# Optimization experiments

Measured on AMD Instinct MI355X. Metric: run time of the kernel, lower is better.

The kernel has to match this reference:

```python
import jax, jax.numpy as jnp
import numpy as np

WINDOW = 8
NUM_HEADS = 16


def setup_inputs() -> dict:
    key = jax.random.key(0)
    k1, k2, k3 = jax.random.split(key, 3)
    B, N_actual, C = 2048, 60, 512
    inputs = jax.random.normal(k1, (B, N_actual, C), dtype=jnp.float32)
    qkv_w = jax.random.normal(k2, (C, 3 * C), dtype=jnp.float32) * 0.05
    qkv_b = jnp.zeros((3 * C,), dtype=jnp.float32)
    proj_w = jax.random.normal(k3, (C, C), dtype=jnp.float32) * 0.05
    proj_b = jnp.zeros((C,), dtype=jnp.float32)
    return {"inputs": inputs, "qkv_w": qkv_w, "qkv_b": qkv_b, "proj_w": proj_w, "proj_b": proj_b}


def reference(inputs, qkv_w, qkv_b, proj_w, proj_b):
    B, N_actual, C = inputs.shape
    H = NUM_HEADS
    hd = C // H
    Nw = WINDOW * WINDOW  # num_tokens_in_window = 64
    pad = Nw - N_actual
    scale = hd ** -0.5

    # pad tokens up to the window size and build the internal padding mask
    x = jnp.pad(inputs, ((0, 0), (0, pad), (0, 0)))  # [B, Nw, C]
    mask = jnp.concatenate(
        [jnp.ones((B, N_actual), dtype=x.dtype), jnp.zeros((B, pad), dtype=x.dtype)], axis=1
    )  # [B, Nw]

    # fused QKV projection
    qkv = x @ qkv_w + qkv_b  # [B, Nw, 3C]
    qkv = qkv.reshape(B, Nw, 3, H, hd).transpose(2, 0, 3, 1, 4)  # [3, B, H, Nw, hd]
    q, k, v = qkv[0] * scale, qkv[1], qkv[2]

    # scaled dot-product attention with additive padding mask
    scores = jnp.einsum("bhnd,bhmd->bhnm", q, k)  # [B, H, Nw, Nw]
    additive_mask = (1.0 - mask)[:, None, None, :] * jnp.asarray(-1e9, scores.dtype)
    attn = jax.nn.softmax(scores + additive_mask, axis=-1)

    out = jnp.einsum("bhnm,bhmd->bhnd", attn, v)  # [B, H, Nw, hd]
    out = out.transpose(0, 2, 1, 3).reshape(B, Nw, C)
    out = out @ proj_w + proj_b
    return out[:, :N_actual, :]
```

## Files before the change

### kernel.cpp

```cpp
#include <hip/hip_runtime.h>

typedef __bf16 bf16x8 __attribute__((ext_vector_type(8)));
typedef float  f32x4  __attribute__((ext_vector_type(4)));

__device__ __forceinline__ f32x4 mfma16(bf16x8 a, bf16x8 b, f32x4 c) {
    return __builtin_amdgcn_mfma_f32_16x16x32_bf16(a, b, c, 0, 0, 0);
}

__device__ __forceinline__ unsigned bpack2(float a, float b) {
    union { __bf16 h[2]; unsigned u; } z;
    z.h[0] = (__bf16)a; z.h[1] = (__bf16)b;
    return z.u;
}

__global__ void kprep(const float* __restrict__ qkvw, const float* __restrict__ qkvb,
                      const float* __restrict__ projw,
                      __bf16* __restrict__ wqkv_t, __bf16* __restrict__ wp_t,
                      float* __restrict__ bias_eff)
{
    const float s = 0.17677669529663687f;
    int idx = blockIdx.x * 256 + threadIdx.x;
    if (idx < 786432) {
        int c = idx >> 9, k = idx & 511;
        float v = qkvw[k * 1536 + c];
        if (c < 512) v *= s;
        wqkv_t[idx] = (__bf16)v;
    } else if (idx < 1048576) {
        int j = idx - 786432;
        int c = j >> 9, k = j & 511;
        wp_t[j] = (__bf16)projw[k * 512 + c];
    } else if (idx < 1050112) {
        int c = idx - 1048576;
        float v = qkvb[c];
        if (c < 512) v *= s;
        bias_eff[c] = v;
    }
}

__global__ __launch_bounds__(512, 2) void kfused8(
    const float*  __restrict__ xin,
    const __bf16* __restrict__ wqkv,
    const float*  __restrict__ bias_eff,
    const __bf16* __restrict__ wp,
    const float*  __restrict__ projb,
    float*        __restrict__ out)
{
    const int b    = blockIdx.x;
    const int tid  = threadIdx.x;
    const int lane = tid & 63;
    const int w    = tid >> 6;
    const int q4   = lane >> 4;
    const int l15  = lane & 15;

    extern __shared__ char smem[];
    char* xs = smem;
    char* wb = smem + 65536 + w * 12288;

    const f32x4 fzero = {0.f, 0.f, 0.f, 0.f};

#pragma unroll
    for (int j = 0; j < 8; ++j) {
        int ci = j * 512 + tid;
        int r  = ci >> 6;
        int k0 = (ci & 63) << 3;
        float4 f0 = make_float4(0.f, 0.f, 0.f, 0.f), f1 = f0;
        if (r < 60) {
            const float4* s4 = reinterpret_cast<const float4*>(
                xin + ((size_t)b * 60 + r) * 512 + k0);
            f0 = s4[0]; f1 = s4[1];
        }
        bf16x8 v;
        v[0]=(__bf16)f0.x; v[1]=(__bf16)f0.y; v[2]=(__bf16)f0.z; v[3]=(__bf16)f0.w;
        v[4]=(__bf16)f1.x; v[5]=(__bf16)f1.y; v[6]=(__bf16)f1.z; v[7]=(__bf16)f1.w;
        int addr = ((((k0 >> 5) << 2) + (r >> 4)) * 64
                    + ((k0 >> 3) & 3) * 16 + (r & 15)) * 16;
        *reinterpret_cast<bf16x8*>(xs + addr) = v;
    }
    __syncthreads();

    unsigned oA[16], oB[16];

    for (int i = 0; i < 2; ++i) {
        const int h = (w << 1) + i;
        __threadfence_block();

        for (int s = 0; s < 3; ++s) {
            const __bf16* wcol = wqkv + ((size_t)(s * 512 + h * 32 + l15) * 512) + q4 * 8;
            f32x4 acc[4][2];
#pragma unroll
            for (int mt = 0; mt < 4; ++mt)
#pragma unroll
                for (int n = 0; n < 2; ++n) acc[mt][n] = fzero;

#pragma unroll
            for (int kk = 0; kk < 16; ++kk) {
                bf16x8 a[4];
#pragma unroll
                for (int mt = 0; mt < 4; ++mt)
                    a[mt] = *reinterpret_cast<const bf16x8*>(
                        xs + (((kk << 2) + mt) * 64 + lane) * 16);
                bf16x8 bw[2];
#pragma unroll
                for (int n = 0; n < 2; ++n)
                    bw[n] = *reinterpret_cast<const bf16x8*>(
                        wcol + (size_t)(n * 16) * 512 + kk * 32);
#pragma unroll
                for (int mt = 0; mt < 4; ++mt)
#pragma unroll
                    for (int n = 0; n < 2; ++n)
                        acc[mt][n] = mfma16(a[mt], bw[n], acc[mt][n]);
            }
            float bs0 = bias_eff[s * 512 + h * 32 + l15];
            float bs1 = bias_eff[s * 512 + h * 32 + 16 + l15];
#pragma unroll
            for (int mt = 0; mt < 4; ++mt)
#pragma unroll
                for (int n = 0; n < 2; ++n)
#pragma unroll
                    for (int reg = 0; reg < 4; ++reg) {
                        float val = acc[mt][n][reg] + (n ? bs1 : bs0);
                        if (s < 2) {
                            int hd = n * 16 + l15;
                            int addr = s * 4096
                                + ((mt * 64 + (hd >> 3) * 16 + q4 * 4 + reg) * 16)
                                + (hd & 7) * 2;
                            *reinterpret_cast<__bf16*>(wb + addr) = (__bf16)val;
                        } else {
                            int key = mt * 16 + q4 * 4 + reg;
                            int g   = ((mt >> 1) << 1) + n;
                            int addr = 8192
                                + ((g * 64 + ((key >> 3) & 3) * 16 + l15) * 16)
                                + (key & 7) * 2;
                            *reinterpret_cast<__bf16*>(wb + addr) = (__bf16)val;
                        }
                    }
        }
        __threadfence_block();

        bf16x8 qa[4], kb[4];
#pragma unroll
        for (int mt = 0; mt < 4; ++mt)
            qa[mt] = *reinterpret_cast<const bf16x8*>(wb + (mt * 64 + lane) * 16);
#pragma unroll
        for (int nt = 0; nt < 4; ++nt)
            kb[nt] = *reinterpret_cast<const bf16x8*>(wb + 4096 + (nt * 64 + lane) * 16);
        f32x4 sc[4][4];
#pragma unroll
        for (int mt = 0; mt < 4; ++mt)
#pragma unroll
            for (int nt = 0; nt < 4; ++nt)
                sc[mt][nt] = mfma16(qa[mt], kb[nt], fzero);

        float inv_rs[4][4];
#pragma unroll
        for (int mt = 0; mt < 4; ++mt)
#pragma unroll
            for (int reg = 0; reg < 4; ++reg) {
                float m0 = fmaxf(fmaxf(sc[mt][0][reg], sc[mt][1][reg]), sc[mt][2][reg]);
                float v3 = (l15 < 12) ? sc[mt][3][reg] : -3.0e38f;
                m0 = fmaxf(m0, v3);
#pragma unroll
                for (int d = 1; d < 16; d <<= 1)
                    m0 = fmaxf(m0, __shfl_xor(m0, d));
                float ssum = 0.f;
#pragma unroll
                for (int nt = 0; nt < 4; ++nt) {
                    float p = (nt == 3 && l15 >= 12) ? 0.f
                              : __expf(sc[mt][nt][reg] - m0);
                    sc[mt][nt][reg] = p;
                    ssum += p;
                }
#pragma unroll
                for (int d = 1; d < 16; d <<= 1)
                    ssum += __shfl_xor(ssum, d);
                inv_rs[mt][reg] = 1.f / ssum;
            }

#pragma unroll
        for (int mt = 0; mt < 4; ++mt)
#pragma unroll
            for (int nt = 0; nt < 4; ++nt)
#pragma unroll
                for (int reg = 0; reg < 4; ++reg) {
                    int addr = (((((nt >> 1) << 2) + mt) * 64)
                                + ((((nt & 1) << 1) + (l15 >> 3)) * 16 + q4 * 4 + reg)) * 16
                               + (l15 & 7) * 2;
                    *reinterpret_cast<__bf16*>(wb + addr) = (__bf16)sc[mt][nt][reg];
                }
        __threadfence_block();

        bf16x8 pa[4][2], vb[2][2];
#pragma unroll
        for (int mt = 0; mt < 4; ++mt)
#pragma unroll
            for (int ks = 0; ks < 2; ++ks)
                pa[mt][ks] = *reinterpret_cast<const bf16x8*>(
                    wb + (((ks << 2) + mt) * 64 + lane) * 16);
#pragma unroll
        for (int ks = 0; ks < 2; ++ks)
#pragma unroll
            for (int n = 0; n < 2; ++n)
                vb[ks][n] = *reinterpret_cast<const bf16x8*>(
                    wb + 8192 + (((ks << 1) + n) * 64 + lane) * 16);
        f32x4 o[4][2];
#pragma unroll
        for (int mt = 0; mt < 4; ++mt)
#pragma unroll
            for (int n = 0; n < 2; ++n) {
                o[mt][n] = mfma16(pa[mt][0], vb[0][n], fzero);
                o[mt][n] = mfma16(pa[mt][1], vb[1][n], o[mt][n]);
            }

#pragma unroll
        for (int mt = 0; mt < 4; ++mt)
#pragma unroll
            for (int n = 0; n < 2; ++n)
#pragma unroll
                for (int rp = 0; rp < 2; ++rp) {
                    unsigned pk = bpack2(o[mt][n][2 * rp]     * inv_rs[mt][2 * rp],
                                         o[mt][n][2 * rp + 1] * inv_rs[mt][2 * rp + 1]);
                    if (i == 0) oA[mt * 4 + n * 2 + rp] = pk;
                    else        oB[mt * 4 + n * 2 + rp] = pk;
                }
    }

    __syncthreads();
    {
        const int h0 = w << 1;
#pragma unroll
        for (int mt = 0; mt < 4; ++mt)
#pragma unroll
            for (int n = 0; n < 2; ++n)
#pragma unroll
                for (int rp = 0; rp < 2; ++rp) {
                    int s0 = ((((h0 << 2) + mt) * 64)
                              + ((n * 2 + (l15 >> 3)) * 16 + q4 * 4 + rp * 2)) * 16
                             + (l15 & 7) * 2;
                    unsigned pa = oA[mt * 4 + n * 2 + rp];
                    unsigned pb = oB[mt * 4 + n * 2 + rp];
                    *reinterpret_cast<unsigned short*>(xs + s0)           = (unsigned short)pa;
                    *reinterpret_cast<unsigned short*>(xs + s0 + 16)      = (unsigned short)(pa >> 16);
                    *reinterpret_cast<unsigned short*>(xs + s0 + 4096)    = (unsigned short)pb;
                    *reinterpret_cast<unsigned short*>(xs + s0 + 4096+16) = (unsigned short)(pb >> 16);
                }
    }
    __syncthreads();

    float* outp = out + (size_t)b * 30720;
    for (int pass = 0; pass < 2; ++pass) {
        const int nt0 = (w << 2) + (pass << 1);
        f32x4 acc[4][2];
#pragma unroll
        for (int mt = 0; mt < 4; ++mt)
#pragma unroll
            for (int n = 0; n < 2; ++n) acc[mt][n] = fzero;

#pragma unroll
        for (int kk = 0; kk < 16; ++kk) {
            bf16x8 a[4];
#pragma unroll
            for (int mt = 0; mt < 4; ++mt)
                a[mt] = *reinterpret_cast<const bf16x8*>(
                    xs + (((kk << 2) + mt) * 64 + lane) * 16);
            bf16x8 bw[2];
#pragma unroll
            for (int n = 0; n < 2; ++n)
                bw[n] = *reinterpret_cast<const bf16x8*>(
                    wp + (size_t)((nt0 + n) * 16 + l15) * 512 + kk * 32 + q4 * 8);
#pragma unroll
            for (int mt = 0; mt < 4; ++mt)
#pragma unroll
                for (int n = 0; n < 2; ++n)
                    acc[mt][n] = mfma16(a[mt], bw[n], acc[mt][n]);
        }
#pragma unroll
        for (int n = 0; n < 2; ++n) {
            int c = (nt0 + n) * 16 + l15;
            float bias = projb[c];
#pragma unroll
            for (int mt = 0; mt < 4; ++mt)
#pragma unroll
                for (int reg = 0; reg < 4; ++reg) {
                    int row = mt * 16 + q4 * 4 + reg;
                    if (row < 60)
                        outp[row * 512 + c] = acc[mt][n][reg] + bias;
                }
        }
    }
}

__global__ __launch_bounds__(256, 1) void ka_fused(
    const float*  __restrict__ xin,
    const __bf16* __restrict__ wqkv,
    const float*  __restrict__ bias_eff,
    char*         __restrict__ aobase)
{
    const int b    = blockIdx.x;
    const int tid  = threadIdx.x;
    const int lane = tid & 63;
    const int w    = tid >> 6;
    const int q4   = lane >> 4;
    const int l15  = lane & 15;

    extern __shared__ char smem[];
    char* xs = smem;
    char* wb = smem + 65536 + w * 12288;

    const f32x4 fzero = {0.f, 0.f, 0.f, 0.f};

#pragma unroll
    for (int j = 0; j < 16; ++j) {
        int ci = j * 256 + tid;
        int r  = ci >> 6;
        int k0 = (ci & 63) << 3;
        float4 f0 = make_float4(0.f, 0.f, 0.f, 0.f), f1 = f0;
        if (r < 60) {
            const float4* s4 = reinterpret_cast<const float4*>(
                xin + ((size_t)b * 60 + r) * 512 + k0);
            f0 = s4[0]; f1 = s4[1];
        }
        bf16x8 v;
        v[0]=(__bf16)f0.x; v[1]=(__bf16)f0.y; v[2]=(__bf16)f0.z; v[3]=(__bf16)f0.w;
        v[4]=(__bf16)f1.x; v[5]=(__bf16)f1.y; v[6]=(__bf16)f1.z; v[7]=(__bf16)f1.w;
        int addr = ((((k0 >> 5) << 2) + (r >> 4)) * 64
                    + ((k0 >> 3) & 3) * 16 + (r & 15)) * 16;
        *reinterpret_cast<bf16x8*>(xs + addr) = v;
    }
    __syncthreads();

    for (int i = 0; i < 4; ++i) {
        const int h = (w << 2) + i;
        __threadfence_block();

        for (int s = 0; s < 3; ++s) {
            const __bf16* wcol = wqkv + ((size_t)(s * 512 + h * 32 + l15) * 512) + q4 * 8;
            f32x4 acc[4][2];
#pragma unroll
            for (int mt = 0; mt < 4; ++mt)
#pragma unroll
                for (int n = 0; n < 2; ++n) acc[mt][n] = fzero;

#pragma unroll
            for (int kk = 0; kk < 16; ++kk) {
                bf16x8 a[4];
#pragma unroll
                for (int mt = 0; mt < 4; ++mt)
                    a[mt] = *reinterpret_cast<const bf16x8*>(
                        xs + (((kk << 2) + mt) * 64 + lane) * 16);
                bf16x8 bw[2];
#pragma unroll
                for (int n = 0; n < 2; ++n)
                    bw[n] = *reinterpret_cast<const bf16x8*>(
                        wcol + (size_t)(n * 16) * 512 + kk * 32);
#pragma unroll
                for (int mt = 0; mt < 4; ++mt)
#pragma unroll
                    for (int n = 0; n < 2; ++n)
                        acc[mt][n] = mfma16(a[mt], bw[n], acc[mt][n]);
            }
            float bs0 = bias_eff[s * 512 + h * 32 + l15];
            float bs1 = bias_eff[s * 512 + h * 32 + 16 + l15];
#pragma unroll
            for (int mt = 0; mt < 4; ++mt)
#pragma unroll
                for (int n = 0; n < 2; ++n)
#pragma unroll
                    for (int reg = 0; reg < 4; ++reg) {
                        float val = acc[mt][n][reg] + (n ? bs1 : bs0);
                        if (s < 2) {
                            int hd = n * 16 + l15;
                            int addr = s * 4096
                                + ((mt * 64 + (hd >> 3) * 16 + q4 * 4 + reg) * 16)
                                + (hd & 7) * 2;
                            *reinterpret_cast<__bf16*>(wb + addr) = (__bf16)val;
                        } else {
                            int key = mt * 16 + q4 * 4 + reg;
                            int g   = ((mt >> 1) << 1) + n;
                            int addr = 8192
                                + ((g * 64 + ((key >> 3) & 3) * 16 + l15) * 16)
                                + (key & 7) * 2;
                            *reinterpret_cast<__bf16*>(wb + addr) = (__bf16)val;
                        }
                    }
        }
        __threadfence_block();

        bf16x8 qa[4], kb[4];
#pragma unroll
        for (int mt = 0; mt < 4; ++mt)
            qa[mt] = *reinterpret_cast<const bf16x8*>(wb + (mt * 64 + lane) * 16);
#pragma unroll
        for (int nt = 0; nt < 4; ++nt)
            kb[nt] = *reinterpret_cast<const bf16x8*>(wb + 4096 + (nt * 64 + lane) * 16);
        f32x4 sc[4][4];
#pragma unroll
        for (int mt = 0; mt < 4; ++mt)
#pragma unroll
            for (int nt = 0; nt < 4; ++nt)
                sc[mt][nt] = mfma16(qa[mt], kb[nt], fzero);

        float inv_rs[4][4];
#pragma unroll
        for (int mt = 0; mt < 4; ++mt)
#pragma unroll
            for (int reg = 0; reg < 4; ++reg) {
                float m0 = fmaxf(fmaxf(sc[mt][0][reg], sc[mt][1][reg]), sc[mt][2][reg]);
                float v3 = (l15 < 12) ? sc[mt][3][reg] : -3.0e38f;
                m0 = fmaxf(m0, v3);
#pragma unroll
                for (int d = 1; d < 16; d <<= 1)
                    m0 = fmaxf(m0, __shfl_xor(m0, d));
                float ssum = 0.f;
#pragma unroll
                for (int nt = 0; nt < 4; ++nt) {
                    float p = (nt == 3 && l15 >= 12) ? 0.f
                              : __expf(sc[mt][nt][reg] - m0);
                    sc[mt][nt][reg] = p;
                    ssum += p;
                }
#pragma unroll
                for (int d = 1; d < 16; d <<= 1)
                    ssum += __shfl_xor(ssum, d);
                inv_rs[mt][reg] = 1.f / ssum;
            }

#pragma unroll
        for (int mt = 0; mt < 4; ++mt)
#pragma unroll
            for (int nt = 0; nt < 4; ++nt)
#pragma unroll
                for (int reg = 0; reg < 4; ++reg) {
                    int addr = (((((nt >> 1) << 2) + mt) * 64)
                                + ((((nt & 1) << 1) + (l15 >> 3)) * 16 + q4 * 4 + reg)) * 16
                               + (l15 & 7) * 2;
                    *reinterpret_cast<__bf16*>(wb + addr) = (__bf16)sc[mt][nt][reg];
                }
        __threadfence_block();

        bf16x8 pa[4][2], vb[2][2];
#pragma unroll
        for (int mt = 0; mt < 4; ++mt)
#pragma unroll
            for (int ks = 0; ks < 2; ++ks)
                pa[mt][ks] = *reinterpret_cast<const bf16x8*>(
                    wb + (((ks << 2) + mt) * 64 + lane) * 16);
#pragma unroll
        for (int ks = 0; ks < 2; ++ks)
#pragma unroll
            for (int n = 0; n < 2; ++n)
                vb[ks][n] = *reinterpret_cast<const bf16x8*>(
                    wb + 8192 + (((ks << 1) + n) * 64 + lane) * 16);
        f32x4 o[4][2];
#pragma unroll
        for (int mt = 0; mt < 4; ++mt)
#pragma unroll
            for (int n = 0; n < 2; ++n) {
                o[mt][n] = mfma16(pa[mt][0], vb[0][n], fzero);
                o[mt][n] = mfma16(pa[mt][1], vb[1][n], o[mt][n]);
            }

        char* aob = aobase + (size_t)b * 122880;
#pragma unroll
        for (int mt = 0; mt < 4; ++mt)
#pragma unroll
            for (int n = 0; n < 2; ++n)
#pragma unroll
                for (int reg = 0; reg < 4; ++reg) {
                    float val = o[mt][n][reg] * inv_rs[mt][reg];
                    int addr = ((((h << 2) + mt) * 64)
                                + ((n * 2 + (l15 >> 3)) * 16 + q4 * 4 + reg)) * 16
                               + (l15 & 7) * 2;
                    *reinterpret_cast<__bf16*>(aob + addr) = (__bf16)val;
                }
    }
}

__global__ __launch_bounds__(256, 2) void kb_proj(
    const __bf16* __restrict__ wp,
    const float*  __restrict__ projb,
    char*         __restrict__ dout)
{
    const int b    = blockIdx.x;
    const int tid  = threadIdx.x;
    const int lane = tid & 63;
    const int w    = tid >> 6;
    const int q4   = lane >> 4;
    const int l15  = lane & 15;
    extern __shared__ char smem[];
    char* aob = dout + (size_t)b * 122880;
    const f32x4 fzero = {0.f, 0.f, 0.f, 0.f};

#pragma unroll
    for (int j = 0; j < 16; ++j) {
        int ci = j * 256 + tid;
        reinterpret_cast<uint4*>(smem)[ci] = reinterpret_cast<const uint4*>(aob)[ci];
    }
    __syncthreads();

    float* outp = reinterpret_cast<float*>(aob);
    for (int pass = 0; pass < 4; ++pass) {
        const int nt0 = pass * 8 + w * 2;
        f32x4 acc[4][2];
#pragma unroll
        for (int mt = 0; mt < 4; ++mt)
#pragma unroll
            for (int n = 0; n < 2; ++n) acc[mt][n] = fzero;

#pragma unroll
        for (int kk = 0; kk < 16; ++kk) {
            bf16x8 a[4];
#pragma unroll
            for (int mt = 0; mt < 4; ++mt)
                a[mt] = *reinterpret_cast<const bf16x8*>(
                    smem + (((kk << 2) + mt) * 64 + lane) * 16);
            bf16x8 bw[2];
#pragma unroll
            for (int n = 0; n < 2; ++n)
                bw[n] = *reinterpret_cast<const bf16x8*>(
                    wp + (size_t)((nt0 + n) * 16 + l15) * 512 + kk * 32 + q4 * 8);
#pragma unroll
            for (int mt = 0; mt < 4; ++mt)
#pragma unroll
                for (int n = 0; n < 2; ++n)
                    acc[mt][n] = mfma16(a[mt], bw[n], acc[mt][n]);
        }
#pragma unroll
        for (int n = 0; n < 2; ++n) {
            int c = (nt0 + n) * 16 + l15;
            float bias = projb[c];
#pragma unroll
            for (int mt = 0; mt < 4; ++mt)
#pragma unroll
                for (int reg = 0; reg < 4; ++reg) {
                    int row = mt * 16 + q4 * 4 + reg;
                    if (row < 60)
                        outp[row * 512 + c] = acc[mt][n][reg] + bias;
                }
        }
    }
}

extern "C" void kernel_launch(void* const* d_in, const int* in_sizes, int n_in,
                              void* d_out, int out_size, void* d_ws, size_t ws_size,
                              hipStream_t stream)
{
    const float* xin   = (const float*)d_in[0];
    const float* qkvw  = (const float*)d_in[1];
    const float* qkvb  = (const float*)d_in[2];
    const float* projw = (const float*)d_in[3];
    const float* projb = (const float*)d_in[4];

    __bf16* wqkv_t   = (__bf16*)d_ws;
    __bf16* wp_t     = wqkv_t + 786432;
    float*  bias_eff = (float*)((char*)d_ws + 2097152);

    kprep<<<dim3(4102), dim3(256), 0, stream>>>(qkvw, qkvb, projw,
                                                wqkv_t, wp_t, bias_eff);

    hipError_t e = hipFuncSetAttribute(reinterpret_cast<const void*>(kfused8),
                                       hipFuncAttributeMaxDynamicSharedMemorySize, 163840);
    if (e == hipSuccess) {
        kfused8<<<dim3(2048), dim3(512), 163840, stream>>>(
            xin, wqkv_t, bias_eff, wp_t, projb, (float*)d_out);
    } else {
        (void)hipFuncSetAttribute(reinterpret_cast<const void*>(ka_fused),
                                  hipFuncAttributeMaxDynamicSharedMemorySize, 114688);
        (void)hipFuncSetAttribute(reinterpret_cast<const void*>(kb_proj),
                                  hipFuncAttributeMaxDynamicSharedMemorySize, 65536);
        ka_fused<<<dim3(2048), dim3(256), 114688, stream>>>(xin, wqkv_t, bias_eff,
                                                            (char*)d_out);
        kb_proj<<<dim3(2048), dim3(256), 65536, stream>>>(wp_t, projb, (char*)d_out);
    }
}
```

Before: 1.123 ms.

## Tile weight transpose prep, merge QKV passes, widen proj tiles, nontemporal IO

Replaces the per-element strided weight transpose with an LDS-tiled transpose kernel so global reads and writes are coalesced. In the fused kernel, the three separate Q/K/V projection passes are merged into one k-loop so each A fragment from LDS is reused across all three weights. The output projection handles four column tiles in a single pass instead of two passes of two. Input loads and output stores use nontemporal hints. The merged QKV loop holds 24 accumulators plus the widened projection accumulators, which raises register pressure and could cut occupancy or cause spills under the 512-thread, 2-block launch bound.

```diff
diff --git a/kernel.cpp b/kernel.cpp
--- a/kernel.cpp
+++ b/kernel.cpp
@@ -13,27 +13,56 @@
     return z.u;
 }
 
-__global__ void kprep(const float* __restrict__ qkvw, const float* __restrict__ qkvb,
-                      const float* __restrict__ projw,
-                      __bf16* __restrict__ wqkv_t, __bf16* __restrict__ wp_t,
-                      float* __restrict__ bias_eff)
+__global__ __launch_bounds__(256) void kprep2(
+    const float* __restrict__ qkvw, const float* __restrict__ qkvb,
+    const float* __restrict__ projw,
+    __bf16* __restrict__ wqkv_t, __bf16* __restrict__ wp_t,
+    float* __restrict__ bias_eff)
 {
+    __shared__ __bf16 tile[64][66];
+    const int bid = blockIdx.x;
+    const int tid = threadIdx.x;
+    const int sub = tid >> 6;
+    const int ln  = tid & 63;
     const float s = 0.17677669529663687f;
-    int idx = blockIdx.x * 256 + threadIdx.x;
-    if (idx < 786432) {
-        int c = idx >> 9, k = idx & 511;
-        float v = qkvw[k * 1536 + c];
-        if (c < 512) v *= s;
-        wqkv_t[idx] = (__bf16)v;
-    } else if (idx < 1048576) {
-        int j = idx - 786432;
-        int c = j >> 9, k = j & 511;
-        wp_t[j] = (__bf16)projw[k * 512 + c];
-    } else if (idx < 1050112) {
-        int c = idx - 1048576;
-        float v = qkvb[c];
-        if (c < 512) v *= s;
-        bias_eff[c] = v;
+
+    if (bid < 192) {
+        int c0 = (bid % 24) * 64;
+        int k0 = (bid / 24) * 64;
+#pragma unroll
+        for (int r = 0; r < 16; ++r) {
+            int kl = r * 4 + sub;
+            int c  = c0 + ln;
+            float v = qkvw[(size_t)(k0 + kl) * 1536 + c];
+            if (c < 512) v *= s;
+            tile[kl][ln] = (__bf16)v;
+        }
+        __syncthreads();
+#pragma unroll
+        for (int r = 0; r < 16; ++r) {
+            int cl = r * 4 + sub;
+            wqkv_t[(size_t)(c0 + cl) * 512 + k0 + ln] = tile[ln][cl];
+        }
+    } else if (bid < 256) {
+        int t = bid - 192;
+        int c0 = (t % 8) * 64, k0 = (t / 8) * 64;
+#pragma unroll
+        for (int r = 0; r < 16; ++r) {
+            int kl = r * 4 + sub;
+            tile[kl][ln] = (__bf16)projw[(size_t)(k0 + kl) * 512 + c0 + ln];
+        }
+        __syncthreads();
+#pragma unroll
+        for (int r = 0; r < 16; ++r) {
+            int cl = r * 4 + sub;
+            wp_t[(size_t)(c0 + cl) * 512 + k0 + ln] = tile[ln][cl];
+        }
+    } else {
+        for (int j = tid; j < 1536; j += 256) {
+            float v = qkvb[j];
+            if (j < 512) v *= s;
+            bias_eff[j] = v;
+        }
     }
 }
 
@@ -63,6 +92,262 @@
         int ci = j * 512 + tid;
         int r  = ci >> 6;
         int k0 = (ci & 63) << 3;
+        f32x4 f0 = fzero, f1 = fzero;
+        if (r < 60) {
+            const f32x4* s4 = reinterpret_cast<const f32x4*>(
+                xin + ((size_t)b * 60 + r) * 512 + k0);
+            f0 = __builtin_nontemporal_load(s4);
+            f1 = __builtin_nontemporal_load(s4 + 1);
+        }
+        bf16x8 v;
+        v[0]=(__bf16)f0[0]; v[1]=(__bf16)f0[1]; v[2]=(__bf16)f0[2]; v[3]=(__bf16)f0[3];
+        v[4]=(__bf16)f1[0]; v[5]=(__bf16)f1[1]; v[6]=(__bf16)f1[2]; v[7]=(__bf16)f1[3];
+        int addr = ((((k0 >> 5) << 2) + (r >> 4)) * 64
+                    + ((k0 >> 3) & 3) * 16 + (r & 15)) * 16;
+        *reinterpret_cast<bf16x8*>(xs + addr) = v;
+    }
+    __syncthreads();
+
+    unsigned oA[16], oB[16];
+
+    for (int i = 0; i < 2; ++i) {
+        const int h = (w << 1) + i;
+        __threadfence_block();
+
+        const __bf16* wbase = wqkv + ((size_t)(h * 32 + l15) * 512) + q4 * 8;
+        f32x4 acc3[3][4][2];
+#pragma unroll
+        for (int s = 0; s < 3; ++s)
+#pragma unroll
+            for (int mt = 0; mt < 4; ++mt)
+#pragma unroll
+                for (int n = 0; n < 2; ++n) acc3[s][mt][n] = fzero;
+
+#pragma unroll
+        for (int kk = 0; kk < 16; ++kk) {
+            bf16x8 a[4];
+#pragma unroll
+            for (int mt = 0; mt < 4; ++mt)
+                a[mt] = *reinterpret_cast<const bf16x8*>(
+                    xs + (((kk << 2) + mt) * 64 + lane) * 16);
+#pragma unroll
+            for (int s = 0; s < 3; ++s) {
+                bf16x8 bw0 = *reinterpret_cast<const bf16x8*>(
+                    wbase + (size_t)s * 262144 + kk * 32);
+                bf16x8 bw1 = *reinterpret_cast<const bf16x8*>(
+                    wbase + (size_t)s * 262144 + 16 * 512 + kk * 32);
+#pragma unroll
+                for (int mt = 0; mt < 4; ++mt) {
+                    acc3[s][mt][0] = mfma16(a[mt], bw0, acc3[s][mt][0]);
+                    acc3[s][mt][1] = mfma16(a[mt], bw1, acc3[s][mt][1]);
+                }
+            }
+        }
+#pragma unroll
+        for (int s = 0; s < 3; ++s) {
+            float bs0 = bias_eff[s * 512 + h * 32 + l15];
+            float bs1 = bias_eff[s * 512 + h * 32 + 16 + l15];
+#pragma unroll
+            for (int mt = 0; mt < 4; ++mt)
+#pragma unroll
+                for (int n = 0; n < 2; ++n)
+#pragma unroll
+                    for (int reg = 0; reg < 4; ++reg) {
+                        float val = acc3[s][mt][n][reg] + (n ? bs1 : bs0);
+                        if (s < 2) {
+                            int hd = n * 16 + l15;
+                            int addr = s * 4096
+                                + ((mt * 64 + (hd >> 3) * 16 + q4 * 4 + reg) * 16)
+                                + (hd & 7) * 2;
+                            *reinterpret_cast<__bf16*>(wb + addr) = (__bf16)val;
+                        } else {
+                            int key = mt * 16 + q4 * 4 + reg;
+                            int g   = ((mt >> 1) << 1) + n;
+                            int addr = 8192
+                                + ((g * 64 + ((key >> 3) & 3) * 16 + l15) * 16)
+                                + (key & 7) * 2;
+                            *reinterpret_cast<__bf16*>(wb + addr) = (__bf16)val;
+                        }
+                    }
+        }
+        __threadfence_block();
+
+        bf16x8 qa[4], kb[4];
+#pragma unroll
+        for (int mt = 0; mt < 4; ++mt)
+            qa[mt] = *reinterpret_cast<const bf16x8*>(wb + (mt * 64 + lane) * 16);
+#pragma unroll
+        for (int nt = 0; nt < 4; ++nt)
+            kb[nt] = *reinterpret_cast<const bf16x8*>(wb + 4096 + (nt * 64 + lane) * 16);
+        f32x4 sc[4][4];
+#pragma unroll
+        for (int mt = 0; mt < 4; ++mt)
+#pragma unroll
+            for (int nt = 0; nt < 4; ++nt)
+                sc[mt][nt] = mfma16(qa[mt], kb[nt], fzero);
+
+        float inv_rs[4][4];
+#pragma unroll
+        for (int mt = 0; mt < 4; ++mt)
+#pragma unroll
+            for (int reg = 0; reg < 4; ++reg) {
+                float m0 = fmaxf(fmaxf(sc[mt][0][reg], sc[mt][1][reg]), sc[mt][2][reg]);
+                float v3 = (l15 < 12) ? sc[mt][3][reg] : -3.0e38f;
+                m0 = fmaxf(m0, v3);
+#pragma unroll
+                for (int d = 1; d < 16; d <<= 1)
+                    m0 = fmaxf(m0, __shfl_xor(m0, d));
+                float ssum = 0.f;
+#pragma unroll
+                for (int nt = 0; nt < 4; ++nt) {
+                    float p = (nt == 3 && l15 >= 12) ? 0.f
+                              : __expf(sc[mt][nt][reg] - m0);
+                    sc[mt][nt][reg] = p;
+                    ssum += p;
+                }
+#pragma unroll
+                for (int d = 1; d < 16; d <<= 1)
+                    ssum += __shfl_xor(ssum, d);
+                inv_rs[mt][reg] = 1.f / ssum;
+            }
+
+#pragma unroll
+        for (int mt = 0; mt < 4; ++mt)
+#pragma unroll
+            for (int nt = 0; nt < 4; ++nt)
+#pragma unroll
+                for (int reg = 0; reg < 4; ++reg) {
+                    int addr = (((((nt >> 1) << 2) + mt) * 64)
+                                + ((((nt & 1) << 1) + (l15 >> 3)) * 16 + q4 * 4 + reg)) * 16
+                               + (l15 & 7) * 2;
+                    *reinterpret_cast<__bf16*>(wb + addr) = (__bf16)sc[mt][nt][reg];
+                }
+        __threadfence_block();
+
+        bf16x8 pa[4][2], vb[2][2];
+#pragma unroll
+        for (int mt = 0; mt < 4; ++mt)
+#pragma unroll
+            for (int ks = 0; ks < 2; ++ks)
+                pa[mt][ks] = *reinterpret_cast<const bf16x8*>(
+                    wb + (((ks << 2) + mt) * 64 + lane) * 16);
+#pragma unroll
+        for (int ks = 0; ks < 2; ++ks)
+#pragma unroll
+            for (int n = 0; n < 2; ++n)
+                vb[ks][n] = *reinterpret_cast<const bf16x8*>(
+                    wb + 8192 + (((ks << 1) + n) * 64 + lane) * 16);
+        f32x4 o[4][2];
+#pragma unroll
+        for (int mt = 0; mt < 4; ++mt)
+#pragma unroll
+            for (int n = 0; n < 2; ++n) {
+                o[mt][n] = mfma16(pa[mt][0], vb[0][n], fzero);
+                o[mt][n] = mfma16(pa[mt][1], vb[1][n], o[mt][n]);
+            }
+
+#pragma unroll
+        for (int mt = 0; mt < 4; ++mt)
+#pragma unroll
+            for (int n = 0; n < 2; ++n)
+#pragma unroll
+                for (int rp = 0; rp < 2; ++rp) {
+                    unsigned pk = bpack2(o[mt][n][2 * rp]     * inv_rs[mt][2 * rp],
+                                         o[mt][n][2 * rp + 1] * inv_rs[mt][2 * rp + 1]);
+                    if (i == 0) oA[mt * 4 + n * 2 + rp] = pk;
+                    else        oB[mt * 4 + n * 2 + rp] = pk;
+                }
+    }
+
+    __syncthreads();
+    {
+        const int h0 = w << 1;
+#pragma unroll
+        for (int mt = 0; mt < 4; ++mt)
+#pragma unroll
+            for (int n = 0; n < 2; ++n)
+#pragma unroll
+                for (int rp = 0; rp < 2; ++rp) {
+                    int s0 = ((((h0 << 2) + mt) * 64)
+                              + ((n * 2 + (l15 >> 3)) * 16 + q4 * 4 + rp * 2)) * 16
+                             + (l15 & 7) * 2;
+                    unsigned pa = oA[mt * 4 + n * 2 + rp];
+                    unsigned pb = oB[mt * 4 + n * 2 + rp];
+                    *reinterpret_cast<unsigned short*>(xs + s0)           = (unsigned short)pa;
+                    *reinterpret_cast<unsigned short*>(xs + s0 + 16)      = (unsigned short)(pa >> 16);
+                    *reinterpret_cast<unsigned short*>(xs + s0 + 4096)    = (unsigned short)pb;
+                    *reinterpret_cast<unsigned short*>(xs + s0 + 4096+16) = (unsigned short)(pb >> 16);
+                }
+    }
+    __syncthreads();
+
+    float* outp = out + (size_t)b * 30720;
+    {
+        f32x4 acc[4][4];
+#pragma unroll
+        for (int mt = 0; mt < 4; ++mt)
+#pragma unroll
+            for (int j = 0; j < 4; ++j) acc[mt][j] = fzero;
+
+#pragma unroll
+        for (int kk = 0; kk < 16; ++kk) {
+            bf16x8 a[4];
+#pragma unroll
+            for (int mt = 0; mt < 4; ++mt)
+                a[mt] = *reinterpret_cast<const bf16x8*>(
+                    xs + (((kk << 2) + mt) * 64 + lane) * 16);
+            bf16x8 bw[4];
+#pragma unroll
+            for (int j = 0; j < 4; ++j)
+                bw[j] = *reinterpret_cast<const bf16x8*>(
+                    wp + (size_t)(((w << 2) + j) * 16 + l15) * 512 + kk * 32 + q4 * 8);
+#pragma unroll
+            for (int mt = 0; mt < 4; ++mt)
+#pragma unroll
+                for (int j = 0; j < 4; ++j)
+                    acc[mt][j] = mfma16(a[mt], bw[j], acc[mt][j]);
+        }
+#pragma unroll
+        for (int j = 0; j < 4; ++j) {
+            int c = ((w << 2) + j) * 16 + l15;
+            float bias = projb[c];
+#pragma unroll
+            for (int mt = 0; mt < 4; ++mt)
+#pragma unroll
+                for (int reg = 0; reg < 4; ++reg) {
+                    int row = mt * 16 + q4 * 4 + reg;
+                    if (row < 60)
+                        __builtin_nontemporal_store(acc[mt][j][reg] + bias,
+                                                    &outp[row * 512 + c]);
+                }
+        }
+    }
+}
+
+__global__ __launch_bounds__(256, 1) void ka_fused(
+    const float*  __restrict__ xin,
+    const __bf16* __restrict__ wqkv,
+    const float*  __restrict__ bias_eff,
+    char*         __restrict__ aobase)
+{
+    const int b    = blockIdx.x;
+    const int tid  = threadIdx.x;
+    const int lane = tid & 63;
+    const int w    = tid >> 6;
+    const int q4   = lane >> 4;
+    const int l15  = lane & 15;
+
+    extern __shared__ char smem[];
+    char* xs = smem;
+    char* wb = smem + 65536 + w * 12288;
+
+    const f32x4 fzero = {0.f, 0.f, 0.f, 0.f};
+
+#pragma unroll
+    for (int j = 0; j < 16; ++j) {
+        int ci = j * 256 + tid;
+        int r  = ci >> 6;
+        int k0 = (ci & 63) << 3;
         float4 f0 = make_float4(0.f, 0.f, 0.f, 0.f), f1 = f0;
         if (r < 60) {
             const float4* s4 = reinterpret_cast<const float4*>(
@@ -78,10 +363,8 @@
     }
     __syncthreads();
 
-    unsigned oA[16], oB[16];
-
-    for (int i = 0; i < 2; ++i) {
-        const int h = (w << 1) + i;
+    for (int i = 0; i < 4; ++i) {
+        const int h = (w << 2) + i;
         __threadfence_block();
 
         for (int s = 0; s < 3; ++s) {
@@ -211,254 +494,6 @@
                 o[mt][n] = mfma16(pa[mt][1], vb[1][n], o[mt][n]);
             }
 
-#pragma unroll
-        for (int mt = 0; mt < 4; ++mt)
-#pragma unroll
-            for (int n = 0; n < 2; ++n)
-#pragma unroll
-                for (int rp = 0; rp < 2; ++rp) {
-                    unsigned pk = bpack2(o[mt][n][2 * rp]     * inv_rs[mt][2 * rp],
-                                         o[mt][n][2 * rp + 1] * inv_rs[mt][2 * rp + 1]);
-                    if (i == 0) oA[mt * 4 + n * 2 + rp] = pk;
-                    else        oB[mt * 4 + n * 2 + rp] = pk;
-                }
-    }
-
-    __syncthreads();
-    {
-        const int h0 = w << 1;
-#pragma unroll
-        for (int mt = 0; mt < 4; ++mt)
-#pragma unroll
-            for (int n = 0; n < 2; ++n)
-#pragma unroll
-                for (int rp = 0; rp < 2; ++rp) {
-                    int s0 = ((((h0 << 2) + mt) * 64)
-                              + ((n * 2 + (l15 >> 3)) * 16 + q4 * 4 + rp * 2)) * 16
-                             + (l15 & 7) * 2;
-                    unsigned pa = oA[mt * 4 + n * 2 + rp];
-                    unsigned pb = oB[mt * 4 + n * 2 + rp];
-                    *reinterpret_cast<unsigned short*>(xs + s0)           = (unsigned short)pa;
-                    *reinterpret_cast<unsigned short*>(xs + s0 + 16)      = (unsigned short)(pa >> 16);
-                    *reinterpret_cast<unsigned short*>(xs + s0 + 4096)    = (unsigned short)pb;
-                    *reinterpret_cast<unsigned short*>(xs + s0 + 4096+16) = (unsigned short)(pb >> 16);
-                }
-    }
-    __syncthreads();
-
-    float* outp = out + (size_t)b * 30720;
-    for (int pass = 0; pass < 2; ++pass) {
-        const int nt0 = (w << 2) + (pass << 1);
-        f32x4 acc[4][2];
-#pragma unroll
-        for (int mt = 0; mt < 4; ++mt)
-#pragma unroll
-            for (int n = 0; n < 2; ++n) acc[mt][n] = fzero;
-
-#pragma unroll
-        for (int kk = 0; kk < 16; ++kk) {
-            bf16x8 a[4];
-#pragma unroll
-            for (int mt = 0; mt < 4; ++mt)
-                a[mt] = *reinterpret_cast<const bf16x8*>(
-                    xs + (((kk << 2) + mt) * 64 + lane) * 16);
-            bf16x8 bw[2];
-#pragma unroll
-            for (int n = 0; n < 2; ++n)
-                bw[n] = *reinterpret_cast<const bf16x8*>(
-                    wp + (size_t)((nt0 + n) * 16 + l15) * 512 + kk * 32 + q4 * 8);
-#pragma unroll
-            for (int mt = 0; mt < 4; ++mt)
-#pragma unroll
-                for (int n = 0; n < 2; ++n)
-                    acc[mt][n] = mfma16(a[mt], bw[n], acc[mt][n]);
-        }
-#pragma unroll
-        for (int n = 0; n < 2; ++n) {
-            int c = (nt0 + n) * 16 + l15;
-            float bias = projb[c];
-#pragma unroll
-            for (int mt = 0; mt < 4; ++mt)
-#pragma unroll
-                for (int reg = 0; reg < 4; ++reg) {
-                    int row = mt * 16 + q4 * 4 + reg;
-                    if (row < 60)
-                        outp[row * 512 + c] = acc[mt][n][reg] + bias;
-                }
-        }
-    }
-}
-
-__global__ __launch_bounds__(256, 1) void ka_fused(
-    const float*  __restrict__ xin,
-    const __bf16* __restrict__ wqkv,
-    const float*  __restrict__ bias_eff,
-    char*         __restrict__ aobase)
-{
-    const int b    = blockIdx.x;
-    const int tid  = threadIdx.x;
-    const int lane = tid & 63;
-    const int w    = tid >> 6;
-    const int q4   = lane >> 4;
-    const int l15  = lane & 15;
-
-    extern __shared__ char smem[];
-    char* xs = smem;
-    char* wb = smem + 65536 + w * 12288;
-
-    const f32x4 fzero = {0.f, 0.f, 0.f, 0.f};
-
-#pragma unroll
-    for (int j = 0; j < 16; ++j) {
-        int ci = j * 256 + tid;
-        int r  = ci >> 6;
-        int k0 = (ci & 63) << 3;
-        float4 f0 = make_float4(0.f, 0.f, 0.f, 0.f), f1 = f0;
-        if (r < 60) {
-            const float4* s4 = reinterpret_cast<const float4*>(
-                xin + ((size_t)b * 60 + r) * 512 + k0);
-            f0 = s4[0]; f1 = s4[1];
-        }
-        bf16x8 v;
-        v[0]=(__bf16)f0.x; v[1]=(__bf16)f0.y; v[2]=(__bf16)f0.z; v[3]=(__bf16)f0.w;
-        v[4]=(__bf16)f1.x; v[5]=(__bf16)f1.y; v[6]=(__bf16)f1.z; v[7]=(__bf16)f1.w;
-        int addr = ((((k0 >> 5) << 2) + (r >> 4)) * 64
-                    + ((k0 >> 3) & 3) * 16 + (r & 15)) * 16;
-        *reinterpret_cast<bf16x8*>(xs + addr) = v;
-    }
-    __syncthreads();
-
-    for (int i = 0; i < 4; ++i) {
-        const int h = (w << 2) + i;
-        __threadfence_block();
-
-        for (int s = 0; s < 3; ++s) {
-            const __bf16* wcol = wqkv + ((size_t)(s * 512 + h * 32 + l15) * 512) + q4 * 8;
-            f32x4 acc[4][2];
-#pragma unroll
-            for (int mt = 0; mt < 4; ++mt)
-#pragma unroll
-                for (int n = 0; n < 2; ++n) acc[mt][n] = fzero;
-
-#pragma unroll
-            for (int kk = 0; kk < 16; ++kk) {
-                bf16x8 a[4];
-#pragma unroll
-                for (int mt = 0; mt < 4; ++mt)
-                    a[mt] = *reinterpret_cast<const bf16x8*>(
-                        xs + (((kk << 2) + mt) * 64 + lane) * 16);
-                bf16x8 bw[2];
-#pragma unroll
-                for (int n = 0; n < 2; ++n)
-                    bw[n] = *reinterpret_cast<const bf16x8*>(
-                        wcol + (size_t)(n * 16) * 512 + kk * 32);
-#pragma unroll
-                for (int mt = 0; mt < 4; ++mt)
-#pragma unroll
-                    for (int n = 0; n < 2; ++n)
-                        acc[mt][n] = mfma16(a[mt], bw[n], acc[mt][n]);
-            }
-            float bs0 = bias_eff[s * 512 + h * 32 + l15];
-            float bs1 = bias_eff[s * 512 + h * 32 + 16 + l15];
-#pragma unroll
-            for (int mt = 0; mt < 4; ++mt)
-#pragma unroll
-                for (int n = 0; n < 2; ++n)
-#pragma unroll
-                    for (int reg = 0; reg < 4; ++reg) {
-                        float val = acc[mt][n][reg] + (n ? bs1 : bs0);
-                        if (s < 2) {
-                            int hd = n * 16 + l15;
-                            int addr = s * 4096
-                                + ((mt * 64 + (hd >> 3) * 16 + q4 * 4 + reg) * 16)
-                                + (hd & 7) * 2;
-                            *reinterpret_cast<__bf16*>(wb + addr) = (__bf16)val;
-                        } else {
-                            int key = mt * 16 + q4 * 4 + reg;
-                            int g   = ((mt >> 1) << 1) + n;
-                            int addr = 8192
-                                + ((g * 64 + ((key >> 3) & 3) * 16 + l15) * 16)
-                                + (key & 7) * 2;
-                            *reinterpret_cast<__bf16*>(wb + addr) = (__bf16)val;
-                        }
-                    }
-        }
-        __threadfence_block();
-
-        bf16x8 qa[4], kb[4];
-#pragma unroll
-        for (int mt = 0; mt < 4; ++mt)
-            qa[mt] = *reinterpret_cast<const bf16x8*>(wb + (mt * 64 + lane) * 16);
-#pragma unroll
-        for (int nt = 0; nt < 4; ++nt)
-            kb[nt] = *reinterpret_cast<const bf16x8*>(wb + 4096 + (nt * 64 + lane) * 16);
-        f32x4 sc[4][4];
-#pragma unroll
-        for (int mt = 0; mt < 4; ++mt)
-#pragma unroll
-            for (int nt = 0; nt < 4; ++nt)
-                sc[mt][nt] = mfma16(qa[mt], kb[nt], fzero);
-
-        float inv_rs[4][4];
-#pragma unroll
-        for (int mt = 0; mt < 4; ++mt)
-#pragma unroll
-            for (int reg = 0; reg < 4; ++reg) {
-                float m0 = fmaxf(fmaxf(sc[mt][0][reg], sc[mt][1][reg]), sc[mt][2][reg]);
-                float v3 = (l15 < 12) ? sc[mt][3][reg] : -3.0e38f;
-                m0 = fmaxf(m0, v3);
-#pragma unroll
-                for (int d = 1; d < 16; d <<= 1)
-                    m0 = fmaxf(m0, __shfl_xor(m0, d));
-                float ssum = 0.f;
-#pragma unroll
-                for (int nt = 0; nt < 4; ++nt) {
-                    float p = (nt == 3 && l15 >= 12) ? 0.f
-                              : __expf(sc[mt][nt][reg] - m0);
-                    sc[mt][nt][reg] = p;
-                    ssum += p;
-                }
-#pragma unroll
-                for (int d = 1; d < 16; d <<= 1)
-                    ssum += __shfl_xor(ssum, d);
-                inv_rs[mt][reg] = 1.f / ssum;
-            }
-
-#pragma unroll
-        for (int mt = 0; mt < 4; ++mt)
-#pragma unroll
-            for (int nt = 0; nt < 4; ++nt)
-#pragma unroll
-                for (int reg = 0; reg < 4; ++reg) {
-                    int addr = (((((nt >> 1) << 2) + mt) * 64)
-                                + ((((nt & 1) << 1) + (l15 >> 3)) * 16 + q4 * 4 + reg)) * 16
-                               + (l15 & 7) * 2;
-                    *reinterpret_cast<__bf16*>(wb + addr) = (__bf16)sc[mt][nt][reg];
-                }
-        __threadfence_block();
-
-        bf16x8 pa[4][2], vb[2][2];
-#pragma unroll
-        for (int mt = 0; mt < 4; ++mt)
-#pragma unroll
-            for (int ks = 0; ks < 2; ++ks)
-                pa[mt][ks] = *reinterpret_cast<const bf16x8*>(
-                    wb + (((ks << 2) + mt) * 64 + lane) * 16);
-#pragma unroll
-        for (int ks = 0; ks < 2; ++ks)
-#pragma unroll
-            for (int n = 0; n < 2; ++n)
-                vb[ks][n] = *reinterpret_cast<const bf16x8*>(
-                    wb + 8192 + (((ks << 1) + n) * 64 + lane) * 16);
-        f32x4 o[4][2];
-#pragma unroll
-        for (int mt = 0; mt < 4; ++mt)
-#pragma unroll
-            for (int n = 0; n < 2; ++n) {
-                o[mt][n] = mfma16(pa[mt][0], vb[0][n], fzero);
-                o[mt][n] = mfma16(pa[mt][1], vb[1][n], o[mt][n]);
-            }
-
         char* aob = aobase + (size_t)b * 122880;
 #pragma unroll
         for (int mt = 0; mt < 4; ++mt)
@@ -554,7 +589,7 @@
     __bf16* wp_t     = wqkv_t + 786432;
     float*  bias_eff = (float*)((char*)d_ws + 2097152);
 
-    kprep<<<dim3(4102), dim3(256), 0, stream>>>(qkvw, qkvb, projw,
+    kprep2<<<dim3(257), dim3(256), 0, stream>>>(qkvw, qkvb, projw,
                                                 wqkv_t, wp_t, bias_eff);
 
     hipError_t e = hipFuncSetAttribute(reinterpret_cast<const void*>(kfused8),
```

Result: faster. 987.5 us (-12.1%).
